# Kernel tuning notes

Hardware: AMD Instinct MI355X
Metric: run time of the kernel (lower is better)

## Reference

```python
import jax, jax.numpy as jnp
import numpy as np

N = 1024   # num_nodes
E = 16384  # num undirected edges (avg degree ~32)
D = 16     # restriction-map (stalk) dimension


def setup_inputs() -> dict:
    rng = np.random.default_rng(0)
    # sample candidate upper-triangular edges, dedupe; np.unique lexsorts, which
    # matches the row-major ordering that torch boolean-mask assignment assumes.
    r = rng.integers(0, N, 6 * E)
    c = rng.integers(0, N, 6 * E)
    m = r < c
    pairs = np.unique(np.stack([r[m], c[m]], axis=1), axis=0)[:E]  # [E, 2]
    assert pairs.shape[0] == E
    row, col = pairs[:, 0], pairs[:, 1]
    edge_index = np.concatenate(
        [np.stack([row, col], 0), np.stack([col, row], 0)], axis=1
    ).astype(np.int64)  # [2, 2E]: first E = triu edges, last E = reversed
    adj = np.zeros((N, N), np.float32)
    adj[row, col] = 1.0
    adj[col, row] = 1.0
    deg = (np.bincount(row, minlength=N) + np.bincount(col, minlength=N)).astype(np.float32)
    maps = jax.random.normal(jax.random.key(0), (2 * E, D, D), dtype=jnp.float32)
    return {
        "adj_mat": jnp.asarray(adj),
        "degrees": jnp.asarray(deg),
        "maps": maps,
        "edge_index": jnp.asarray(edge_index),
    }


def reference(adj_mat, degrees, maps, edge_index):
    num_edges = maps.shape[0] // 2
    num_nodes = adj_mat.shape[0]
    d = maps.shape[1]
    md = maps.shape[-1]

    src = edge_index[0]  # row endpoint of every directed edge block, [2E]
    # per-directed-edge Gram block: maps_e^T @ maps_e -> [2E, md, md]
    blocks = jnp.einsum('eij,eik->ejk', maps, maps)
    # diagonal block per node = sum of its incident edge blocks (row-sum of adj_mat_maps)
    maps_diag = jax.ops.segment_sum(blocks, src, num_segments=num_nodes)  # [N, md, md]

    maps_from = maps[:num_edges]
    maps_to = maps[num_edges:]
    # off-diagonal upper-triangular blocks: maps_from^T @ maps_to -> [E, md, md]
    maps_triu = jnp.einsum('eij,eik->ejk', maps_from, maps_to)

    row = edge_index[0, :num_edges]
    col = edge_index[1, :num_edges]
    dinv = (degrees * d + 1.0) ** -0.5  # [N]
    maps_triu = dinv[row, None, None] * maps_triu * dinv[col, None, None]
    maps_diag = dinv[:, None, None] * maps_diag * dinv[:, None, None]
    maps_tril = jnp.swapaxes(maps_triu, 1, 2)

    # assemble dense block Laplacian [N, N, md, md]
    L = jnp.zeros((num_nodes, num_nodes, md, md), maps.dtype)
    L = L.at[row, col].set(-maps_triu)
    L = L.at[col, row].set(-maps_tril)
    diag_idx = jnp.arange(num_nodes)
    L = L.at[diag_idx, diag_idx].set(maps_diag)
    # interleave block dims: (n, i, m, j) -> [N*md, N*md]
    return L.transpose(0, 2, 1, 3).reshape(num_nodes * md, num_nodes * md)
```

## Files before the change

### kernel.cpp

```cpp
#include <hip/hip_runtime.h>


#define NN 1024
#define EE 16384
#define DD 16
#define LD (NN * DD)

__global__ __launch_bounds__(256) void lap_edges_kernel(
    const float* __restrict__ maps,
    const float* __restrict__ degrees,
    const int*   __restrict__ edge_index,
    float* __restrict__ out)
{
    __shared__ float Mf[256];
    __shared__ float Mt[256];

    const int e = blockIdx.x;
    const int t = threadIdx.x;
    const int j = t >> 4;
    const int k = t & 15;

    Mf[t] = maps[(size_t)e * 256 + t];
    const int  src = edge_index[e];
    const bool tri = (e < EE);
    int dst = 0;
    if (tri) {
        Mt[t] = maps[(size_t)(e + EE) * 256 + t];
        dst = edge_index[2 * EE + e];
    }
    __syncthreads();

    const float dinv_s = rsqrtf(degrees[src] * 16.0f + 1.0f);

    float b = 0.0f;
    #pragma unroll
    for (int i = 0; i < 16; ++i)
        b += Mf[i * 16 + j] * Mf[i * 16 + k];
    atomicAdd(&out[(size_t)(src * 16 + j) * LD + (src * 16 + k)],
              b * dinv_s * dinv_s);

    if (tri) {
        const float dinv_d = rsqrtf(degrees[dst] * 16.0f + 1.0f);
        const float s = dinv_s * dinv_d;
        float tjk = 0.0f, tkj = 0.0f;
        #pragma unroll
        for (int i = 0; i < 16; ++i) {
            const float fj = Mf[i * 16 + j];
            const float fk = Mf[i * 16 + k];
            const float gj = Mt[i * 16 + j];
            const float gk = Mt[i * 16 + k];
            tjk += fj * gk;
            tkj += fk * gj;
        }
        out[(size_t)(src * 16 + j) * LD + (dst * 16 + k)] = -s * tjk;
        out[(size_t)(dst * 16 + j) * LD + (src * 16 + k)] = -s * tkj;
    }
}

extern "C" void kernel_launch(void* const* d_in, const int* in_sizes, int n_in,
                              void* d_out, int out_size, void* d_ws, size_t ws_size,
                              hipStream_t stream) {
    const float* degrees    = (const float*)d_in[1];
    const float* maps       = (const float*)d_in[2];
    const int*   edge_index = (const int*)d_in[3];
    float* out = (float*)d_out;

    hipMemsetAsync(out, 0, (size_t)out_size * sizeof(float), stream);

    lap_edges_kernel<<<2 * EE, 256, 0, stream>>>(maps, degrees, edge_index, out);
}
```

Measured before the change: 1.098 ms.

## Replace diagonal atomics with per-node CSR gather and custom zero fill

Builds a per-node CSR list of incident directed edges in workspace, then computes each node's diagonal block in a single block that sums the Gram products of all its edges. This removes the float atomicAdds on the diagonal blocks and halves the edge-block grid. The memset is replaced by a float4 grid-stride zero kernel. In exchange there are three extra launches, the diagonal blocks run a serial loop with two syncs per edge, and the CSR assumes degree at most 128 and reads the degree from the float input.

```diff
diff --git a/kernel.cpp b/kernel.cpp
--- a/kernel.cpp
+++ b/kernel.cpp
@@ -3,45 +3,53 @@
 
 #define NN 1024
 #define EE 16384
-#define DD 16
-#define LD (NN * DD)
+#define LD (NN * 16)
+#define CSR_STRIDE 128
 
-__global__ __launch_bounds__(256) void lap_edges_kernel(
+
+__global__ __launch_bounds__(256) void zero_counters(int* __restrict__ cnt) {
+    cnt[blockIdx.x * 256 + threadIdx.x] = 0;
+}
+
+__global__ __launch_bounds__(256) void build_csr(const int* __restrict__ edge_index,
+                                                 int* __restrict__ cnt,
+                                                 int* __restrict__ csr) {
+    const int e = blockIdx.x * 256 + threadIdx.x;
+    const int n = edge_index[e];
+    const int slot = atomicAdd(&cnt[n], 1);
+    csr[n * CSR_STRIDE + slot] = e;
+}
+
+__global__ __launch_bounds__(256) void zero_fill(float4* __restrict__ out, long n4) {
+    const float4 z = make_float4(0.f, 0.f, 0.f, 0.f);
+    long i = (long)blockIdx.x * 256 + threadIdx.x;
+    const long stride = (long)gridDim.x * 256;
+    for (; i < n4; i += stride)
+        out[i] = z;
+}
+
+__global__ __launch_bounds__(256) void lap_blocks(
     const float* __restrict__ maps,
     const float* __restrict__ degrees,
     const int*   __restrict__ edge_index,
+    const int*   __restrict__ csr,
     float* __restrict__ out)
 {
     __shared__ float Mf[256];
     __shared__ float Mt[256];
-
-    const int e = blockIdx.x;
     const int t = threadIdx.x;
     const int j = t >> 4;
     const int k = t & 15;
+    const int b = blockIdx.x;
 
-    Mf[t] = maps[(size_t)e * 256 + t];
-    const int  src = edge_index[e];
-    const bool tri = (e < EE);
-    int dst = 0;
-    if (tri) {
-        Mt[t] = maps[(size_t)(e + EE) * 256 + t];
-        dst = edge_index[2 * EE + e];
-    }
-    __syncthreads();
-
-    const float dinv_s = rsqrtf(degrees[src] * 16.0f + 1.0f);
-
-    float b = 0.0f;
-    #pragma unroll
-    for (int i = 0; i < 16; ++i)
-        b += Mf[i * 16 + j] * Mf[i * 16 + k];
-    atomicAdd(&out[(size_t)(src * 16 + j) * LD + (src * 16 + k)],
-              b * dinv_s * dinv_s);
-
-    if (tri) {
-        const float dinv_d = rsqrtf(degrees[dst] * 16.0f + 1.0f);
-        const float s = dinv_s * dinv_d;
+    if (b < EE) {
+        const int src = edge_index[b];
+        const int dst = edge_index[2 * EE + b];
+        Mf[t] = maps[(size_t)b * 256 + t];
+        Mt[t] = maps[(size_t)(b + EE) * 256 + t];
+        __syncthreads();
+        const float s = rsqrtf(degrees[src] * 16.0f + 1.0f) *
+                        rsqrtf(degrees[dst] * 16.0f + 1.0f);
         float tjk = 0.0f, tkj = 0.0f;
         #pragma unroll
         for (int i = 0; i < 16; ++i) {
@@ -54,6 +62,21 @@
         }
         out[(size_t)(src * 16 + j) * LD + (dst * 16 + k)] = -s * tjk;
         out[(size_t)(dst * 16 + j) * LD + (src * 16 + k)] = -s * tkj;
+    } else {
+        const int n = b - EE;
+        const int deg = (int)degrees[n];
+        float acc = 0.0f;
+        for (int q = 0; q < deg; ++q) {
+            const int e = csr[n * CSR_STRIDE + q];
+            __syncthreads();
+            Mf[t] = maps[(size_t)e * 256 + t];
+            __syncthreads();
+            #pragma unroll
+            for (int i = 0; i < 16; ++i)
+                acc += Mf[i * 16 + j] * Mf[i * 16 + k];
+        }
+        const float di = rsqrtf(degrees[n] * 16.0f + 1.0f);
+        out[(size_t)(n * 16 + j) * LD + (n * 16 + k)] = acc * di * di;
     }
 }
 
@@ -65,7 +88,11 @@
     const int*   edge_index = (const int*)d_in[3];
     float* out = (float*)d_out;
 
-    hipMemsetAsync(out, 0, (size_t)out_size * sizeof(float), stream);
+    int* cnt = (int*)d_ws;
+    int* csr = cnt + 1024;
 
-    lap_edges_kernel<<<2 * EE, 256, 0, stream>>>(maps, degrees, edge_index, out);
+    zero_counters<<<NN / 256, 256, 0, stream>>>(cnt);
+    build_csr<<<2 * EE / 256, 256, 0, stream>>>(edge_index, cnt, csr);
+    zero_fill<<<4096, 256, 0, stream>>>((float4*)out, (long)out_size / 4);
+    lap_blocks<<<EE + NN, 256, 0, stream>>>(maps, degrees, edge_index, csr, out);
 }
```

After: 1.266 ms. 15.3% more time.

## Fuse zero-fill and block computation into a dense row-wise writer via edge index map

Applied to the files above, without the earlier changes.

Replaces the full-output memset followed by scattered per-edge writes and atomics with a dense edge-id lookup table (short per node pair) built in workspace. A fused kernel then walks each output block-row segment and writes every float4 exactly once, either zero, the diagonal block, or an off-diagonal Gram product computed on the fly. This removes the separate 1 GiB zero pass and the atomics, at the cost of a serial per-row diagonal accumulation over all 1024 columns and redundant reads of the maps inside the fill kernel.

```diff
diff --git a/kernel.cpp b/kernel.cpp
--- a/kernel.cpp
+++ b/kernel.cpp
@@ -3,57 +3,94 @@
 
 #define NN 1024
 #define EE 16384
-#define DD 16
-#define LD (NN * DD)
+#define LDim 16384
 
-__global__ __launch_bounds__(256) void lap_edges_kernel(
+
+__global__ __launch_bounds__(256) void zero_idx(int4* __restrict__ idx4) {
+    idx4[blockIdx.x * 256 + threadIdx.x] = make_int4(0, 0, 0, 0);
+}
+
+__global__ __launch_bounds__(256) void scatter_idx(const int* __restrict__ edge_index,
+                                                   short* __restrict__ idx) {
+    const int e = blockIdx.x * 256 + threadIdx.x;
+    const int r = edge_index[e];
+    const int c = edge_index[2 * EE + e];
+    idx[r * NN + c] = (short)(e + 1);
+    idx[c * NN + r] = (short)(-(e + 1));
+}
+
+__global__ __launch_bounds__(256) void fused_fill(
     const float* __restrict__ maps,
     const float* __restrict__ degrees,
-    const int*   __restrict__ edge_index,
+    const short* __restrict__ idx,
     float* __restrict__ out)
 {
-    __shared__ float Mf[256];
-    __shared__ float Mt[256];
+    __shared__ short sIdx[NN];
+    __shared__ float sDiag[256];
+    const int t = threadIdx.x;
+    const int r = blockIdx.x >> 2;
+    const int seg = blockIdx.x & 3;
 
-    const int e = blockIdx.x;
-    const int t = threadIdx.x;
-    const int j = t >> 4;
-    const int k = t & 15;
+    ((int2*)sIdx)[t] = ((const int2*)(idx + (size_t)r * NN))[t];
+    __syncthreads();
 
-    Mf[t] = maps[(size_t)e * 256 + t];
-    const int  src = edge_index[e];
-    const bool tri = (e < EE);
-    int dst = 0;
-    if (tri) {
-        Mt[t] = maps[(size_t)(e + EE) * 256 + t];
-        dst = edge_index[2 * EE + e];
+    const float dinv_r = rsqrtf(degrees[r] * 16.0f + 1.0f);
+
+    if (seg == (r >> 8)) {
+        const int j = t >> 4, k = t & 15;
+        float acc = 0.0f;
+        for (int c2 = 0; c2 < NN; ++c2) {
+            const int id = sIdx[c2];
+            if (id != 0) {
+                const int m = (id > 0) ? (id - 1) : (-id - 1 + EE);
+                const float* M = maps + (size_t)m * 256;
+                #pragma unroll
+                for (int i = 0; i < 16; ++i)
+                    acc += M[i * 16 + j] * M[i * 16 + k];
+            }
+        }
+        sDiag[t] = acc * dinv_r * dinv_r;
     }
     __syncthreads();
 
-    const float dinv_s = rsqrtf(degrees[src] * 16.0f + 1.0f);
-
-    float b = 0.0f;
-    #pragma unroll
-    for (int i = 0; i < 16; ++i)
-        b += Mf[i * 16 + j] * Mf[i * 16 + k];
-    atomicAdd(&out[(size_t)(src * 16 + j) * LD + (src * 16 + k)],
-              b * dinv_s * dinv_s);
-
-    if (tri) {
-        const float dinv_d = rsqrtf(degrees[dst] * 16.0f + 1.0f);
-        const float s = dinv_s * dinv_d;
-        float tjk = 0.0f, tkj = 0.0f;
-        #pragma unroll
-        for (int i = 0; i < 16; ++i) {
-            const float fj = Mf[i * 16 + j];
-            const float fk = Mf[i * 16 + k];
-            const float gj = Mt[i * 16 + j];
-            const float gk = Mt[i * 16 + k];
-            tjk += fj * gk;
-            tkj += fk * gj;
+    const int k4 = (t & 3) * 4;
+    const int cb_local = t >> 2;
+    for (int j = 0; j < 16; ++j) {
+        const size_t rowbase = (size_t)(r * 16 + j) * LDim + (size_t)seg * 4096;
+        for (int chunk = 0; chunk < 4; ++chunk) {
+            const int c = seg * 256 + chunk * 64 + cb_local;
+            const int id = sIdx[c];
+            float4 v = make_float4(0.f, 0.f, 0.f, 0.f);
+            if (c == r) {
+                v = *(const float4*)&sDiag[j * 16 + k4];
+            } else if (id != 0) {
+                const int e = (id > 0) ? id - 1 : -id - 1;
+                const float* A = maps + (size_t)e * 256;
+                const float* B = A + (size_t)EE * 256;
+                float4 acc = make_float4(0.f, 0.f, 0.f, 0.f);
+                if (id > 0) {
+                    #pragma unroll
+                    for (int i = 0; i < 16; ++i) {
+                        const float  aj = A[i * 16 + j];
+                        const float4 b4 = *(const float4*)&B[i * 16 + k4];
+                        acc.x += aj * b4.x; acc.y += aj * b4.y;
+                        acc.z += aj * b4.z; acc.w += aj * b4.w;
+                    }
+                } else {
+                    #pragma unroll
+                    for (int i = 0; i < 16; ++i) {
+                        const float  bj = B[i * 16 + j];
+                        const float4 a4 = *(const float4*)&A[i * 16 + k4];
+                        acc.x += bj * a4.x; acc.y += bj * a4.y;
+                        acc.z += bj * a4.z; acc.w += bj * a4.w;
+                    }
+                }
+                const float s = -dinv_r * rsqrtf(degrees[c] * 16.0f + 1.0f);
+                v.x = s * acc.x; v.y = s * acc.y;
+                v.z = s * acc.z; v.w = s * acc.w;
+            }
+            *(float4*)&out[rowbase + (size_t)chunk * 1024 + t * 4] = v;
         }
-        out[(size_t)(src * 16 + j) * LD + (dst * 16 + k)] = -s * tjk;
-        out[(size_t)(dst * 16 + j) * LD + (src * 16 + k)] = -s * tkj;
     }
 }
 
@@ -64,8 +101,9 @@
     const float* maps       = (const float*)d_in[2];
     const int*   edge_index = (const int*)d_in[3];
     float* out = (float*)d_out;
+    short* idx = (short*)d_ws;
 
-    hipMemsetAsync(out, 0, (size_t)out_size * sizeof(float), stream);
-
-    lap_edges_kernel<<<2 * EE, 256, 0, stream>>>(maps, degrees, edge_index, out);
+    zero_idx<<<512, 256, 0, stream>>>((int4*)idx);
+    scatter_idx<<<EE / 256, 256, 0, stream>>>(edge_index, idx);
+    fused_fill<<<4 * NN, 256, 0, stream>>>(maps, degrees, idx, out);
 }
```

New measurement: 1.529 ms. 1.39x slower.

## Replace full memset with masked zero-fill using an edge index map

Applied to the files above, without the earlier changes.

Builds a dense N×N short index map of edge ids in the workspace, then fuses into one launch a masked zero-fill that skips blocks later written by edges or diagonals, the off-diagonal edge blocks, and per-node diagonal blocks gathered from the index map instead of atomics. The goal is to avoid writing the full 1 GiB output twice (memset plus scatter) and to remove atomic adds. In exchange it adds two small pre-kernels and a serial 1024-column scan per node with uncoalesced global reads of maps for the diagonal blocks.

```diff
diff --git a/kernel.cpp b/kernel.cpp
--- a/kernel.cpp
+++ b/kernel.cpp
@@ -3,46 +3,66 @@
 
 #define NN 1024
 #define EE 16384
-#define DD 16
-#define LD (NN * DD)
+#define LDim 16384
+#define FILL_WGS 4096
 
-__global__ __launch_bounds__(256) void lap_edges_kernel(
+typedef float vf4 __attribute__((ext_vector_type(4)));
+
+__global__ __launch_bounds__(256) void zero_idx(int4* __restrict__ idx4) {
+    idx4[blockIdx.x * 256 + threadIdx.x] = make_int4(0, 0, 0, 0);
+}
+
+__global__ __launch_bounds__(256) void scatter_idx(const int* __restrict__ ei,
+                                                   short* __restrict__ idx) {
+    const int e = blockIdx.x * 256 + threadIdx.x;
+    const int r = ei[e];
+    const int c = ei[2 * EE + e];
+    idx[r * NN + c] = (short)(e + 1);
+    idx[c * NN + r] = (short)(-(e + 1));
+}
+
+__global__ __launch_bounds__(256) void lap_main(
     const float* __restrict__ maps,
     const float* __restrict__ degrees,
     const int*   __restrict__ edge_index,
+    const short* __restrict__ idx,
     float* __restrict__ out)
 {
-    __shared__ float Mf[256];
-    __shared__ float Mt[256];
+    const int t = threadIdx.x;
+    const int b = blockIdx.x;
 
-    const int e = blockIdx.x;
-    const int t = threadIdx.x;
-    const int j = t >> 4;
-    const int k = t & 15;
-
-    Mf[t] = maps[(size_t)e * 256 + t];
-    const int  src = edge_index[e];
-    const bool tri = (e < EE);
-    int dst = 0;
-    if (tri) {
+    if (b < FILL_WGS) {
+        __shared__ short sIdx[NN];
+        const int r = b >> 2, seg = b & 3;
+        ((int2*)sIdx)[t] = ((const int2*)(idx + (size_t)r * NN))[t];
+        __syncthreads();
+        const int cb = seg * 256 + (t >> 2);
+        const bool m0 = (sIdx[cb      ] == 0) & (cb       != r);
+        const bool m1 = (sIdx[cb +  64] == 0) & (cb +  64 != r);
+        const bool m2 = (sIdx[cb + 128] == 0) & (cb + 128 != r);
+        const bool m3 = (sIdx[cb + 192] == 0) & (cb + 192 != r);
+        const vf4 z = {0.f, 0.f, 0.f, 0.f};
+        for (int j = 0; j < 16; ++j) {
+            vf4* p = (vf4*)(out + (size_t)(r * 16 + j) * LDim
+                                + (size_t)seg * 4096) + t;
+            if (m0) __builtin_nontemporal_store(z, p);
+            if (m1) __builtin_nontemporal_store(z, p + 256);
+            if (m2) __builtin_nontemporal_store(z, p + 512);
+            if (m3) __builtin_nontemporal_store(z, p + 768);
+        }
+    } else if (b < FILL_WGS + EE) {
+        const int e = b - FILL_WGS;
+        __shared__ float Mf[256];
+        __shared__ float Mt[256];
+        Mf[t] = maps[(size_t)e * 256 + t];
         Mt[t] = maps[(size_t)(e + EE) * 256 + t];
-        dst = edge_index[2 * EE + e];
-    }
-    __syncthreads();
-
-    const float dinv_s = rsqrtf(degrees[src] * 16.0f + 1.0f);
-
-    float b = 0.0f;
-    #pragma unroll
-    for (int i = 0; i < 16; ++i)
-        b += Mf[i * 16 + j] * Mf[i * 16 + k];
-    atomicAdd(&out[(size_t)(src * 16 + j) * LD + (src * 16 + k)],
-              b * dinv_s * dinv_s);
-
-    if (tri) {
-        const float dinv_d = rsqrtf(degrees[dst] * 16.0f + 1.0f);
-        const float s = dinv_s * dinv_d;
-        float tjk = 0.0f, tkj = 0.0f;
+        const int src = edge_index[e];
+        const int dst = edge_index[2 * EE + e];
+        __syncthreads();
+        const float s = rsqrtf(degrees[src] * 16.f + 1.f) *
+                        rsqrtf(degrees[dst] * 16.f + 1.f);
+        const int j = t >> 4, k = t & 15;
+        float tjk = 0.f, tkj = 0.f;
         #pragma unroll
         for (int i = 0; i < 16; ++i) {
             const float fj = Mf[i * 16 + j];
@@ -52,8 +72,27 @@
             tjk += fj * gk;
             tkj += fk * gj;
         }
-        out[(size_t)(src * 16 + j) * LD + (dst * 16 + k)] = -s * tjk;
-        out[(size_t)(dst * 16 + j) * LD + (src * 16 + k)] = -s * tkj;
+        out[(size_t)(src * 16 + j) * LDim + dst * 16 + k] = -s * tjk;
+        out[(size_t)(dst * 16 + j) * LDim + src * 16 + k] = -s * tkj;
+    } else {
+        const int n = b - FILL_WGS - EE;
+        __shared__ short sIdx2[NN];
+        ((int2*)sIdx2)[t] = ((const int2*)(idx + (size_t)n * NN))[t];
+        __syncthreads();
+        const int j = t >> 4, k = t & 15;
+        float acc = 0.f;
+        for (int c = 0; c < NN; ++c) {
+            const int id = sIdx2[c];
+            if (id != 0) {
+                const int m = (id > 0) ? (id - 1) : (-id - 1 + EE);
+                const float* __restrict__ M = maps + (size_t)m * 256;
+                #pragma unroll
+                for (int i = 0; i < 16; ++i)
+                    acc += M[i * 16 + j] * M[i * 16 + k];
+            }
+        }
+        const float di = rsqrtf(degrees[n] * 16.f + 1.f);
+        out[(size_t)(n * 16 + j) * LDim + n * 16 + k] = acc * di * di;
     }
 }
 
@@ -64,8 +103,10 @@
     const float* maps       = (const float*)d_in[2];
     const int*   edge_index = (const int*)d_in[3];
     float* out = (float*)d_out;
+    short* idx = (short*)d_ws;
 
-    hipMemsetAsync(out, 0, (size_t)out_size * sizeof(float), stream);
-
-    lap_edges_kernel<<<2 * EE, 256, 0, stream>>>(maps, degrees, edge_index, out);
+    zero_idx<<<512, 256, 0, stream>>>((int4*)idx);
+    scatter_idx<<<EE / 256, 256, 0, stream>>>(edge_index, idx);
+    lap_main<<<FILL_WGS + EE + NN, 256, 0, stream>>>(maps, degrees, edge_index,
+                                                     idx, out);
 }
```

Measured after the change: 1.226 ms. 11.7% more time.
